# Optimization experiments

Measured on AMD Instinct MI355X. Metric: run time of the kernel, lower is better.

The kernel has to match this reference:

```python
import jax, jax.numpy as jnp
from jax import lax
import numpy as np

DN = ('NCDHW', 'OIDHW', 'NCDHW')


def _conv3(x, w, b):
    # standard 3x3x3 conv, stride 1, pad 1
    y = lax.conv_general_dilated(x, w, (1, 1, 1), ((1, 1), (1, 1), (1, 1)), dimension_numbers=DN)
    return y + b[None, :, None, None, None]


def _bn(x, gamma, beta, eps=1e-5):
    # training-mode batchnorm over (N, D, H, W), biased variance (torch semantics)
    mean = jnp.mean(x, axis=(0, 2, 3, 4), keepdims=True)
    var = jnp.var(x, axis=(0, 2, 3, 4), keepdims=True)
    return gamma[None, :, None, None, None] * (x - mean) * lax.rsqrt(var + eps) + beta[None, :, None, None, None]


def _deform_conv(x, off, w):
    # ConvOffset3d: one scalar offset per deformable group shifting the temporal (D)
    # sampling position of every kernel tap; linear interpolation along D, zero padding.
    N, C, D, H, W = x.shape
    G = off.shape[1]
    cpg = C // G
    offc = jnp.repeat(off, cpg, axis=1)                        # [N,C,D,H,W]
    base = offc + jnp.arange(D, dtype=x.dtype)[None, None, :, None, None]
    out = None
    for kd in range(3):                                        # 3 temporal taps
        pos = base + (kd - 1)                                  # fractional sample pos along D
        f0 = jnp.floor(pos)
        frac = pos - f0
        i0 = f0.astype(jnp.int32)
        i1 = i0 + 1
        m0 = ((i0 >= 0) & (i0 < D)).astype(x.dtype)
        m1 = ((i1 >= 0) & (i1 < D)).astype(x.dtype)
        g = (jnp.take_along_axis(x, jnp.clip(i0, 0, D - 1), axis=2) * ((1.0 - frac) * m0)
             + jnp.take_along_axis(x, jnp.clip(i1, 0, D - 1), axis=2) * (frac * m1))
        # the D-shift for tap kd is already baked into g -> conv with kernel (1,3,3)
        y = lax.conv_general_dilated(g, w[:, :, kd:kd + 1], (1, 1, 1), ((0, 0), (1, 1), (1, 1)), dimension_numbers=DN)
        out = y if out is None else out + y
    return out


def setup_inputs() -> dict:
    key = jax.random.key(0)
    ks = jax.random.split(key, 4)
    C, cpg = 64, 8
    N, D, H, W = 8, 16, 56, 56
    G = C // cpg
    s = 1.0 / np.sqrt(C * 27).astype(np.float32)
    x = jax.random.normal(ks[0], (N, C, D, H, W), jnp.float32)
    w_off = jax.random.normal(ks[1], (G, C, 3, 3, 3), jnp.float32) * s
    b_off = jnp.zeros((G,), jnp.float32)
    w1 = jax.random.normal(ks[2], (C, C, 3, 3, 3), jnp.float32) * s
    w2 = jax.random.normal(ks[3], (C, C, 3, 3, 3), jnp.float32) * s
    b2 = jnp.zeros((C,), jnp.float32)
    return dict(x=x, w_off=w_off, b_off=b_off, w1=w1, w2=w2, b2=b2,
                bn1_gamma=jnp.ones((C,), jnp.float32), bn1_beta=jnp.zeros((C,), jnp.float32),
                bn2_gamma=jnp.ones((C,), jnp.float32), bn2_beta=jnp.zeros((C,), jnp.float32))


def reference(x, w_off, b_off, w1, w2, b2, bn1_gamma, bn1_beta, bn2_gamma, bn2_beta):
    off = _conv3(x, w_off, b_off)               # [N, G, D, H, W]
    out = _deform_conv(x, off, w1)              # deformable conv (no bias)
    out = jax.nn.relu(_bn(out, bn1_gamma, bn1_beta))
    out = _conv3(out, w2, b2)
    out = _bn(out, bn2_gamma, bn2_beta) + x     # residual
    out = jax.nn.relu(out)
    return (out, off)
```

## Files before the change

kernel.cpp:

```cpp
#include <hip/hip_runtime.h>

#define HW 3136
#define DHW 50176
#define NEL 25690112
#define CNT 401408.0f

typedef __attribute__((ext_vector_type(8))) short          short8;
typedef __attribute__((ext_vector_type(8))) unsigned short ushort8;
typedef __attribute__((ext_vector_type(4))) float          f32x4;

__device__ __forceinline__ unsigned f2bf(float f) {
    union { float f; unsigned u; } v; v.f = f;
    return (v.u + 0x7FFFu + ((v.u >> 16) & 1u)) >> 16;
}
__device__ __forceinline__ float bf2f(unsigned u) {
    union { unsigned u; float f; } v; v.u = u << 16;
    return v.f;
}
__device__ __forceinline__ unsigned cvt_pk_bf16(float lo, float hi) {
    unsigned r;
    asm("v_cvt_pk_bf16_f32 %0, %1, %2" : "=v"(r) : "v"(lo), "v"(hi));
    return r;
}

__device__ __forceinline__ void xcd_decode(int& h, int& d, int& n) {
    const int bid = blockIdx.x + 56 * (blockIdx.y + 16 * blockIdx.z);
    const int swz = (bid & 7) * 896 + (bid >> 3);
    h = swz % 56;
    const int dn = swz / 56;
    d = dn & 15;
    n = dn >> 4;
}

__global__ __launch_bounds__(256) void k_transpose(
    const float* __restrict__ x, unsigned short* __restrict__ xt)
{
    __shared__ unsigned lds[4][64 * 36];
    const int d = blockIdx.x, n = blockIdx.y, z = blockIdx.z;
    const int wave = threadIdx.x >> 6, lane = threadIdx.x & 63;
    const float* xb = x + (size_t)n * 64 * DHW + d * HW;
    unsigned short* xtb = xt + (size_t)n * DHW * 64;
    unsigned* L = lds[wave];

    for (int c = z * 7 + wave; c < z * 7 + 7 && c < 49; c += 4) {
        const int P = c * 64;
#pragma unroll 4
        for (int cp = 0; cp < 32; ++cp) {
            const float a = xb[(size_t)(2 * cp) * DHW + P + lane];
            const float b = xb[(size_t)(2 * cp + 1) * DHW + P + lane];
            L[lane * 36 + cp] = cvt_pk_bf16(a, b);
        }
#pragma unroll
        for (int k = 0; k < 8; ++k) {
            const int r = (lane >> 3) + 8 * k;
            const uint4 v = *(const uint4*)&L[r * 36 + 4 * (lane & 7)];
            *(uint4*)((char*)xtb + ((size_t)(P + r) * 16 + d) * 128 + (lane & 7) * 16) = v;
        }
    }
}

__global__ __launch_bounds__(256) void k_wprep(
    const float* __restrict__ w_off, const float* __restrict__ w1,
    const float* __restrict__ w2, unsigned short* __restrict__ BtO,
    unsigned short* __restrict__ Bt1, unsigned short* __restrict__ Bt2)
{
    const int i = blockIdx.x * 256 + threadIdx.x;
    if (i < 27648) {
        const int tap = i / 1024, r = i - tap * 1024;
        const int ks = r >> 9, r3 = r & 511, lane = r3 >> 3, e = r3 & 7;
        const int row = lane & 15;
        const int ci  = ks * 32 + (lane >> 4) * 8 + e;
        BtO[i] = (row < 8) ? (unsigned short)f2bf(w_off[(row * 64 + ci) * 27 + tap]) : 0;
    }
    if (i < 110592) {
        const int tap = i / 4096, r = i - tap * 4096;
        const int rg = r >> 10, r2 = r & 1023;
        const int ks = r2 >> 9, r3 = r2 & 511, lane = r3 >> 3, e = r3 & 7;
        const int co = rg * 16 + (lane & 15);
        const int ci = ks * 32 + (lane >> 4) * 8 + e;
        Bt1[i] = (unsigned short)f2bf(w1[(co * 64 + ci) * 27 + tap]);
        Bt2[i] = (unsigned short)f2bf(w2[(co * 64 + ci) * 27 + tap]);
    }
}

template<int NCO, bool BN, bool DIN>
__global__ __launch_bounds__((NCO == 8) ? 256 : 512) void k_conv(
    const unsigned short* __restrict__ src, const unsigned short* __restrict__ Bt,
    const float* __restrict__ bias, const float* __restrict__ scv,
    const float* __restrict__ shv, float* __restrict__ dst)
{
    constexpr int NT = (NCO == 8) ? 256 : 512;
    __shared__ unsigned short A[538 * 72];
    int h, d, n;
    xcd_decode(h, d, n);
    const int tid = threadIdx.x;
    const int wave = tid >> 6, lane = tid & 63, lm = lane & 15, quad = lane >> 4;
    const int k8 = tid & 7;

    float scr[8], shr[8];
    if constexpr (BN) {
#pragma unroll
        for (int e = 0; e < 8; ++e) { scr[e] = scv[k8 * 8 + e]; shr[e] = shv[k8 * 8 + e]; }
    }

    const unsigned short* snb = DIN ? (src + (size_t)n * DHW * 64)
                                    : (src + (size_t)(n * 16) * HW * 64);

    for (int c = tid; c < 4176; c += NT) {
        const int idx = c >> 3;
        const int row = idx / 58, px = idx - row * 58;
        const int kd = row / 3, kh = row - kd * 3;
        const int dq = d + kd - 1, hq = h + kh - 1, wq = px - 1;
        uint4 pk = {0u, 0u, 0u, 0u};
        if (((unsigned)dq < 16u) & ((unsigned)hq < 56u) & ((unsigned)wq < 56u)) {
            const size_t off = DIN ? (((size_t)(hq * 56 + wq) * 16 + dq) * 64)
                                   : (((size_t)dq * HW + hq * 56 + wq) * 64);
            const ushort8 val = *(const ushort8*)(snb + off + k8 * 8);
            if constexpr (BN) {
                float f[8];
#pragma unroll
                for (int e = 0; e < 8; ++e)
                    f[e] = fmaxf(fmaf(bf2f(val[e]), scr[e], shr[e]), 0.f);
                pk.x = cvt_pk_bf16(f[0], f[1]);
                pk.y = cvt_pk_bf16(f[2], f[3]);
                pk.z = cvt_pk_bf16(f[4], f[5]);
                pk.w = cvt_pk_bf16(f[6], f[7]);
            } else {
                pk = *(const uint4*)&val;
            }
        }
        *(uint4*)&A[(size_t)idx * 72 + k8 * 8] = pk;
    }
    __syncthreads();

    constexpr int NFm = (NCO == 8) ? 1 : 2;
    const int mf0 = (NCO == 8) ? wave : (wave & 1) * 2;
    const int nf0 = (NCO == 8) ? 0 : (wave >> 1);

    f32x4 acc[NFm];
#pragma unroll
    for (int i = 0; i < NFm; ++i) acc[i] = (f32x4){0.f, 0.f, 0.f, 0.f};

    constexpr unsigned BSTR = (NCO == 8) ? 1024u : 4096u;
    const unsigned short* Btb = (NCO == 8) ? Bt : (Bt + (unsigned)nf0 * 1024);
    unsigned boff = (unsigned)lane * 8;
    short8 bc0 = *(const short8*)(Btb + boff);
    short8 bc1 = *(const short8*)(Btb + boff + 512);
    boff += BSTR;
    unsigned arow = (unsigned)(mf0 * 16 + lm) * 72 + quad * 8;

#pragma unroll 1
    for (int r9 = 0; r9 < 9; ++r9) {
#pragma unroll
        for (int kw = 0; kw < 3; ++kw) {
            const bool more = (kw < 2) | (r9 < 8);
            short8 bn0, bn1;
            if (more) {
                bn0 = *(const short8*)(Btb + boff);
                bn1 = *(const short8*)(Btb + boff + 512);
            }
            const unsigned ab = arow + kw * 72;
            short8 a0[NFm], a1[NFm];
#pragma unroll
            for (int mf = 0; mf < NFm; ++mf) {
                a0[mf] = *(const short8*)&A[ab + mf * 1152];
                a1[mf] = *(const short8*)&A[ab + mf * 1152 + 32];
            }
#pragma unroll
            for (int mf = 0; mf < NFm; ++mf)
                acc[mf] = __builtin_amdgcn_mfma_f32_16x16x32_bf16(a0[mf], bc0, acc[mf], 0, 0, 0);
#pragma unroll
            for (int mf = 0; mf < NFm; ++mf)
                acc[mf] = __builtin_amdgcn_mfma_f32_16x16x32_bf16(a1[mf], bc1, acc[mf], 0, 0, 0);
            if (more) {
                bc0 = bn0; bc1 = bn1;
                boff += BSTR;
            }
        }
        arow += 58 * 72;
    }

    __syncthreads();
    float* E = (float*)A;
    constexpr int CSTR = (NCO == 64) ? 65 : 17;
#pragma unroll
    for (int mf = 0; mf < NFm; ++mf)
#pragma unroll
        for (int r = 0; r < 4; ++r) {
            const int mm = (mf0 + mf) * 16 + quad * 4 + r;
            if (mm < 56) E[mm * CSTR + nf0 * 16 + lm] = acc[mf][r];
        }
    __syncthreads();
    for (int f = tid; f < 56 * NCO; f += NT) {
        const int co = f / 56, w0 = f - co * 56;
        dst[((size_t)(n * NCO + co) * 16 + d) * HW + h * 56 + w0] = E[w0 * CSTR + co] + bias[co];
    }
}

__global__ __launch_bounds__(512) void k_deform(
    const unsigned short* __restrict__ xt, const float* __restrict__ offo,
    const unsigned short* __restrict__ Bt, unsigned short* __restrict__ out1)
{
    __shared__ unsigned short A[538 * 72];
    int h, d, n;
    xcd_decode(h, d, n);
    const int tid = threadIdx.x;
    const int wave = tid >> 6, lane = tid & 63, lm = lane & 15, quad = lane >> 4;

    float pv[3];
#pragma unroll
    for (int it = 0; it < 3; ++it) {
        const int c = tid + it * 512;
        float p = 0.f;
        if (c < 1392) {
            const int g = c & 7, pix = c >> 3;
            const int hq3 = pix / 58, px = pix - hq3 * 58;
            const int habs = h + hq3 - 1, wq = px - 1;
            if (((unsigned)habs < 56u) & ((unsigned)wq < 56u))
                p = offo[((size_t)(n * 8 + g) * 16 + d) * HW + habs * 56 + wq] + (float)d;
        }
        pv[it] = p;
    }

#pragma unroll
    for (int it = 0; it < 3; ++it) {
        const int c = tid + it * 512;
        if (c >= 1392) break;
        const int g = c & 7, pix = c >> 3;
        const int hq3 = pix / 58, px = pix - hq3 * 58;
        const int habs = h + hq3 - 1, wq = px - 1;
        uint4 p0 = {0u,0u,0u,0u}, p1 = {0u,0u,0u,0u}, p2 = {0u,0u,0u,0u};
        if (((unsigned)habs < 56u) & ((unsigned)wq < 56u)) {
            const float p = pv[it];
            const float fl = floorf(p);
            const float fr = p - fl;
            const int i0 = (int)fl;
            const unsigned short* cb = xt + ((size_t)n * HW + habs * 56 + wq) * (16 * 64) + g * 8;
            float sv[4][8], m[4];
#pragma unroll
            for (int j = 0; j < 4; ++j) {
                const int dj = i0 - 1 + j;
                const bool ok = (unsigned)dj < 16u;
                m[j] = ok ? 1.f : 0.f;
                const ushort8 v = *(const ushort8*)(cb + (size_t)(ok ? dj : 0) * 64);
#pragma unroll
                for (int e = 0; e < 8; ++e) sv[j][e] = bf2f(v[e]);
            }
            const float fi = 1.f - fr;
            const float w0a = fi * m[0], w0b = fr * m[1];
            const float w1a = fi * m[1], w1b = fr * m[2];
            const float w2a = fi * m[2], w2b = fr * m[3];
            float a0[8], a1[8], a2[8];
#pragma unroll
            for (int e = 0; e < 8; ++e) {
                a0[e] = fmaf(sv[1][e], w0b, sv[0][e] * w0a);
                a1[e] = fmaf(sv[2][e], w1b, sv[1][e] * w1a);
                a2[e] = fmaf(sv[3][e], w2b, sv[2][e] * w2a);
            }
            p0.x = cvt_pk_bf16(a0[0], a0[1]); p0.y = cvt_pk_bf16(a0[2], a0[3]);
            p0.z = cvt_pk_bf16(a0[4], a0[5]); p0.w = cvt_pk_bf16(a0[6], a0[7]);
            p1.x = cvt_pk_bf16(a1[0], a1[1]); p1.y = cvt_pk_bf16(a1[2], a1[3]);
            p1.z = cvt_pk_bf16(a1[4], a1[5]); p1.w = cvt_pk_bf16(a1[6], a1[7]);
            p2.x = cvt_pk_bf16(a2[0], a2[1]); p2.y = cvt_pk_bf16(a2[2], a2[3]);
            p2.z = cvt_pk_bf16(a2[4], a2[5]); p2.w = cvt_pk_bf16(a2[6], a2[7]);
        }
        const int sl = hq3 * 58 + px;
        *(uint4*)&A[(size_t)(sl          ) * 72 + g * 8] = p0;
        *(uint4*)&A[(size_t)(sl + 3 * 58 ) * 72 + g * 8] = p1;
        *(uint4*)&A[(size_t)(sl + 6 * 58 ) * 72 + g * 8] = p2;
    }
    __syncthreads();

    const int mf0 = (wave & 1) * 2, nf0 = wave >> 1;
    f32x4 acc[2];
    acc[0] = (f32x4){0.f, 0.f, 0.f, 0.f};
    acc[1] = (f32x4){0.f, 0.f, 0.f, 0.f};

    const unsigned short* Btb = Bt + (unsigned)nf0 * 1024;
    unsigned boff = (unsigned)lane * 8;
    short8 bc0 = *(const short8*)(Btb + boff);
    short8 bc1 = *(const short8*)(Btb + boff + 512);
    boff += 4096u;
    unsigned arow = (unsigned)(mf0 * 16 + lm) * 72 + quad * 8;

#pragma unroll 1
    for (int r9 = 0; r9 < 9; ++r9) {
#pragma unroll
        for (int kw = 0; kw < 3; ++kw) {
            const bool more = (kw < 2) | (r9 < 8);
            short8 bn0, bn1;
            if (more) {
                bn0 = *(const short8*)(Btb + boff);
                bn1 = *(const short8*)(Btb + boff + 512);
            }
            const unsigned ab = arow + kw * 72;
            const short8 a00 = *(const short8*)&A[ab];
            const short8 a01 = *(const short8*)&A[ab + 1152];
            const short8 a10 = *(const short8*)&A[ab + 32];
            const short8 a11 = *(const short8*)&A[ab + 1152 + 32];
            acc[0] = __builtin_amdgcn_mfma_f32_16x16x32_bf16(a00, bc0, acc[0], 0, 0, 0);
            acc[1] = __builtin_amdgcn_mfma_f32_16x16x32_bf16(a01, bc0, acc[1], 0, 0, 0);
            acc[0] = __builtin_amdgcn_mfma_f32_16x16x32_bf16(a10, bc1, acc[0], 0, 0, 0);
            acc[1] = __builtin_amdgcn_mfma_f32_16x16x32_bf16(a11, bc1, acc[1], 0, 0, 0);
            if (more) {
                bc0 = bn0; bc1 = bn1;
                boff += 4096u;
            }
        }
        arow += 58 * 72;
    }

    __syncthreads();
#pragma unroll
    for (int mf = 0; mf < 2; ++mf)
#pragma unroll
        for (int r = 0; r < 4; ++r) {
            const int mm = (mf0 + mf) * 16 + quad * 4 + r;
            if (mm < 56)
                A[mm * 72 + nf0 * 16 + lm] = (unsigned short)f2bf(acc[mf][r]);
        }
    __syncthreads();
    const size_t pixb = ((size_t)(n * 16) + d) * HW + h * 56;
    if (tid < 448) {
        const int px = tid >> 3, kk = tid & 7;
        *(uint4*)(out1 + (pixb + px) * 64 + kk * 8) = *(const uint4*)&A[px * 72 + kk * 8];
    }
}

__global__ __launch_bounds__(256) void k_stats_bf16(
    const unsigned short* __restrict__ src, float* __restrict__ sums, float* __restrict__ sqs)
{
    const int c4 = threadIdx.x & 15, part = threadIdx.x >> 4;
    const size_t base = (size_t)blockIdx.x * 1024;
    float s[4] = {0.f, 0.f, 0.f, 0.f}, q[4] = {0.f, 0.f, 0.f, 0.f};
#pragma unroll 4
    for (int i = 0; i < 64; ++i) {
        const size_t pix = base + part + (size_t)i * 16;
        const uint2 v = *(const uint2*)(src + pix * 64 + c4 * 4);
        const float f0 = bf2f(v.x & 0xffffu), f1 = bf2f(v.x >> 16);
        const float f2 = bf2f(v.y & 0xffffu), f3 = bf2f(v.y >> 16);
        s[0] += f0; q[0] = fmaf(f0, f0, q[0]);
        s[1] += f1; q[1] = fmaf(f1, f1, q[1]);
        s[2] += f2; q[2] = fmaf(f2, f2, q[2]);
        s[3] += f3; q[3] = fmaf(f3, f3, q[3]);
    }
    __shared__ float S[64], Q[64];
    if (threadIdx.x < 64) { S[threadIdx.x] = 0.f; Q[threadIdx.x] = 0.f; }
    __syncthreads();
#pragma unroll
    for (int e = 0; e < 4; ++e) {
        atomicAdd(&S[c4 * 4 + e], s[e]);
        atomicAdd(&Q[c4 * 4 + e], q[e]);
    }
    __syncthreads();
    if (threadIdx.x < 64) {
        atomicAdd(&sums[threadIdx.x], S[threadIdx.x]);
        atomicAdd(&sqs[threadIdx.x],  Q[threadIdx.x]);
    }
}

__global__ __launch_bounds__(256) void k_stats(
    const float* __restrict__ src, float* __restrict__ sums, float* __restrict__ sqs)
{
    const int c = blockIdx.x, n = blockIdx.y;
    const float* p = src + ((size_t)n * 64 + c) * DHW;
    float s = 0.f, q = 0.f;
    for (int i = threadIdx.x; i < DHW; i += 256) {
        const float v = p[i];
        s += v; q = fmaf(v, v, q);
    }
    for (int o = 32; o > 0; o >>= 1) {
        s += __shfl_down(s, o);
        q += __shfl_down(q, o);
    }
    __shared__ float ls[4], lq[4];
    const int wv = threadIdx.x >> 6, lane = threadIdx.x & 63;
    if (lane == 0) { ls[wv] = s; lq[wv] = q; }
    __syncthreads();
    if (threadIdx.x == 0) {
        atomicAdd(&sums[c], ls[0] + ls[1] + ls[2] + ls[3]);
        atomicAdd(&sqs[c],  lq[0] + lq[1] + lq[2] + lq[3]);
    }
}

__global__ void k_finalize(const float* __restrict__ sums, const float* __restrict__ sqs,
                           const float* __restrict__ gamma, const float* __restrict__ beta,
                           float* __restrict__ scale, float* __restrict__ shift)
{
    const int c = threadIdx.x;
    const float mean = sums[c] / CNT;
    const float var  = sqs[c] / CNT - mean * mean;
    const float sc   = gamma[c] * rsqrtf(var + 1e-5f);
    scale[c] = sc;
    shift[c] = fmaf(-mean, sc, beta[c]);
}

__global__ __launch_bounds__(256) void k_residual(
    float4* __restrict__ dst, const float4* __restrict__ raw,
    const float4* __restrict__ x,
    const float* __restrict__ scale, const float* __restrict__ shift)
{
    const int i = blockIdx.x * 256 + threadIdx.x;
    const int c = (i / 12544) & 63;
    const float sc = scale[c], sh = shift[c];
    float4 v = raw[i];
    const float4 xv = x[i];
    v.x = fmaxf(fmaf(v.x, sc, sh) + xv.x, 0.f);
    v.y = fmaxf(fmaf(v.y, sc, sh) + xv.y, 0.f);
    v.z = fmaxf(fmaf(v.z, sc, sh) + xv.z, 0.f);
    v.w = fmaxf(fmaf(v.w, sc, sh) + xv.w, 0.f);
    dst[i] = v;
}

extern "C" void kernel_launch(void* const* d_in, const int* in_sizes, int n_in,
                              void* d_out, int out_size, void* d_ws, size_t ws_size,
                              hipStream_t stream) {
    const float* x     = (const float*)d_in[0];
    const float* w_off = (const float*)d_in[1];
    const float* b_off = (const float*)d_in[2];
    const float* w1    = (const float*)d_in[3];
    const float* w2    = (const float*)d_in[4];
    const float* b2    = (const float*)d_in[5];
    const float* g1    = (const float*)d_in[6];
    const float* be1   = (const float*)d_in[7];
    const float* g2    = (const float*)d_in[8];
    const float* be2   = (const float*)d_in[9];

    float* out     = (float*)d_out;
    float* off_out = out + NEL;
    unsigned short* out1 = (unsigned short*)d_out;
    unsigned short* wb   = (unsigned short*)(out + 13000000);
    unsigned short* BtO  = wb;
    unsigned short* Bt1  = BtO + 27648;
    unsigned short* Bt2  = Bt1 + 110592;

    unsigned short* xt  = (unsigned short*)d_ws;
    float*          raw = (float*)d_ws;
    float*          st  = (float*)d_ws + NEL;

    hipMemsetAsync(st, 0, 512 * sizeof(float), stream);

    k_transpose<<<dim3(16, 8, 7), 256, 0, stream>>>(x, xt);
    k_wprep<<<432, 256, 0, stream>>>(w_off, w1, w2, BtO, Bt1, Bt2);

    const dim3 cgrid(56, 16, 8);
    k_conv<8, false, true><<<cgrid, 256, 0, stream>>>(xt, BtO, b_off, nullptr, nullptr, off_out);
    k_deform<<<cgrid, 512, 0, stream>>>(xt, off_out, Bt1, out1);

    k_stats_bf16<<<392, 256, 0, stream>>>(out1, st + 0, st + 64);
    k_finalize<<<1, 64, 0, stream>>>(st + 0, st + 64, g1, be1, st + 128, st + 192);

    k_conv<64, true, false><<<cgrid, 512, 0, stream>>>(out1, Bt2, b2, st + 128, st + 192, raw);

    k_stats<<<dim3(64, 8), 256, 0, stream>>>(raw, st + 256, st + 320);
    k_finalize<<<1, 64, 0, stream>>>(st + 256, st + 320, g2, be2, st + 384, st + 448);
    k_residual<<<25088, 256, 0, stream>>>((float4*)out, (const float4*)raw, (const float4*)x, st + 384, st + 448);
}
```

Before: 751.9 us.

## Fuse batchnorm statistics into conv epilogues and split offset-conv K across waves

Removes the separate k_stats_bf16 and k_stats passes by computing per-channel sums and sums of squares in the epilogues of the deformable conv and the second conv. Each epilogue reduces over 8 lanes with shuffles and then does global atomics. The offset conv now runs with 512 threads and splits the K dimension across two wave groups, summing the two partials through shared memory. The tile load loop is also rewritten into a fixed 9-row unrolled pattern. This saves two full reads of the large intermediates, at the cost of many more global atomics and a slightly different floating-point summation order.

```diff
diff --git a/kernel.cpp b/kernel.cpp
--- a/kernel.cpp
+++ b/kernel.cpp
@@ -84,12 +84,12 @@
 }
 
 template<int NCO, bool BN, bool DIN>
-__global__ __launch_bounds__((NCO == 8) ? 256 : 512) void k_conv(
+__global__ __launch_bounds__(512) void k_conv(
     const unsigned short* __restrict__ src, const unsigned short* __restrict__ Bt,
     const float* __restrict__ bias, const float* __restrict__ scv,
-    const float* __restrict__ shv, float* __restrict__ dst)
-{
-    constexpr int NT = (NCO == 8) ? 256 : 512;
+    const float* __restrict__ shv, float* __restrict__ dst,
+    float* __restrict__ osum, float* __restrict__ osq)
+{
     __shared__ unsigned short A[538 * 72];
     int h, d, n;
     xcd_decode(h, d, n);
@@ -106,13 +106,15 @@
     const unsigned short* snb = DIN ? (src + (size_t)n * DHW * 64)
                                     : (src + (size_t)(n * 16) * HW * 64);
 
-    for (int c = tid; c < 4176; c += NT) {
-        const int idx = c >> 3;
-        const int row = idx / 58, px = idx - row * 58;
-        const int kd = row / 3, kh = row - kd * 3;
-        const int dq = d + kd - 1, hq = h + kh - 1, wq = px - 1;
+    const int spx = tid >> 3;
+    const int wq  = spx - 1;
+    const bool pxok = (tid < 464) & ((unsigned)wq < 56u);
+#pragma unroll
+    for (int row = 0; row < 9; ++row) {
+        const int kd = row / 3, kh = row - (row / 3) * 3;
+        const int dq = d + kd - 1, hq = h + kh - 1;
         uint4 pk = {0u, 0u, 0u, 0u};
-        if (((unsigned)dq < 16u) & ((unsigned)hq < 56u) & ((unsigned)wq < 56u)) {
+        if (pxok & ((unsigned)dq < 16u) & ((unsigned)hq < 56u)) {
             const size_t off = DIN ? (((size_t)(hq * 56 + wq) * 16 + dq) * 64)
                                    : (((size_t)dq * HW + hq * 56 + wq) * 64);
             const ushort8 val = *(const ushort8*)(snb + off + k8 * 8);
@@ -129,77 +131,115 @@
                 pk = *(const uint4*)&val;
             }
         }
-        *(uint4*)&A[(size_t)idx * 72 + k8 * 8] = pk;
+        if (tid < 464) *(uint4*)&A[(size_t)(row * 58 + spx) * 72 + k8 * 8] = pk;
     }
     __syncthreads();
 
-    constexpr int NFm = (NCO == 8) ? 1 : 2;
-    const int mf0 = (NCO == 8) ? wave : (wave & 1) * 2;
-    const int nf0 = (NCO == 8) ? 0 : (wave >> 1);
-
-    f32x4 acc[NFm];
-#pragma unroll
-    for (int i = 0; i < NFm; ++i) acc[i] = (f32x4){0.f, 0.f, 0.f, 0.f};
-
-    constexpr unsigned BSTR = (NCO == 8) ? 1024u : 4096u;
-    const unsigned short* Btb = (NCO == 8) ? Bt : (Bt + (unsigned)nf0 * 1024);
-    unsigned boff = (unsigned)lane * 8;
-    short8 bc0 = *(const short8*)(Btb + boff);
-    short8 bc1 = *(const short8*)(Btb + boff + 512);
-    boff += BSTR;
-    unsigned arow = (unsigned)(mf0 * 16 + lm) * 72 + quad * 8;
-
+    if constexpr (NCO == 8) {
+        const int ksw = wave >> 2, mf = wave & 3;
+        f32x4 acc = (f32x4){0.f, 0.f, 0.f, 0.f};
+        const unsigned short* Btb = Bt + ksw * 512;
+        unsigned boff = (unsigned)lane * 8;
+        short8 bc = *(const short8*)(Btb + boff);
+        boff += 1024u;
+        unsigned arow = (unsigned)(mf * 16 + lm) * 72 + quad * 8 + ksw * 32;
 #pragma unroll 1
-    for (int r9 = 0; r9 < 9; ++r9) {
-#pragma unroll
-        for (int kw = 0; kw < 3; ++kw) {
-            const bool more = (kw < 2) | (r9 < 8);
-            short8 bn0, bn1;
-            if (more) {
-                bn0 = *(const short8*)(Btb + boff);
-                bn1 = *(const short8*)(Btb + boff + 512);
-            }
-            const unsigned ab = arow + kw * 72;
-            short8 a0[NFm], a1[NFm];
-#pragma unroll
-            for (int mf = 0; mf < NFm; ++mf) {
-                a0[mf] = *(const short8*)&A[ab + mf * 1152];
-                a1[mf] = *(const short8*)&A[ab + mf * 1152 + 32];
-            }
-#pragma unroll
-            for (int mf = 0; mf < NFm; ++mf)
-                acc[mf] = __builtin_amdgcn_mfma_f32_16x16x32_bf16(a0[mf], bc0, acc[mf], 0, 0, 0);
-#pragma unroll
-            for (int mf = 0; mf < NFm; ++mf)
-                acc[mf] = __builtin_amdgcn_mfma_f32_16x16x32_bf16(a1[mf], bc1, acc[mf], 0, 0, 0);
-            if (more) {
-                bc0 = bn0; bc1 = bn1;
-                boff += BSTR;
-            }
-        }
-        arow += 58 * 72;
-    }
-
-    __syncthreads();
-    float* E = (float*)A;
-    constexpr int CSTR = (NCO == 64) ? 65 : 17;
-#pragma unroll
-    for (int mf = 0; mf < NFm; ++mf)
+        for (int r9 = 0; r9 < 9; ++r9) {
+#pragma unroll
+            for (int kw = 0; kw < 3; ++kw) {
+                const bool more = (kw < 2) | (r9 < 8);
+                short8 bn;
+                if (more) bn = *(const short8*)(Btb + boff);
+                const short8 a = *(const short8*)&A[arow + kw * 72];
+                acc = __builtin_amdgcn_mfma_f32_16x16x32_bf16(a, bc, acc, 0, 0, 0);
+                if (more) { bc = bn; boff += 1024u; }
+            }
+            arow += 58 * 72;
+        }
+        __syncthreads();
+        float* E = (float*)A;
 #pragma unroll
         for (int r = 0; r < 4; ++r) {
-            const int mm = (mf0 + mf) * 16 + quad * 4 + r;
-            if (mm < 56) E[mm * CSTR + nf0 * 16 + lm] = acc[mf][r];
-        }
-    __syncthreads();
-    for (int f = tid; f < 56 * NCO; f += NT) {
-        const int co = f / 56, w0 = f - co * 56;
-        dst[((size_t)(n * NCO + co) * 16 + d) * HW + h * 56 + w0] = E[w0 * CSTR + co] + bias[co];
+            const int mm = mf * 16 + quad * 4 + r;
+            if (mm < 56) E[ksw * 952 + mm * 17 + lm] = acc[r];
+        }
+        __syncthreads();
+        if (lane < 56) {
+            const float v = E[lane * 17 + wave] + E[952 + lane * 17 + wave] + bias[wave];
+            dst[((size_t)(n * 8 + wave) * 16 + d) * HW + h * 56 + lane] = v;
+        }
+    } else {
+        const int mf0 = (wave & 1) * 2, nf0 = wave >> 1;
+        f32x4 acc[2];
+        acc[0] = (f32x4){0.f, 0.f, 0.f, 0.f};
+        acc[1] = (f32x4){0.f, 0.f, 0.f, 0.f};
+
+        const unsigned short* Btb = Bt + (unsigned)nf0 * 1024;
+        unsigned boff = (unsigned)lane * 8;
+        short8 bc0 = *(const short8*)(Btb + boff);
+        short8 bc1 = *(const short8*)(Btb + boff + 512);
+        boff += 4096u;
+        unsigned arow = (unsigned)(mf0 * 16 + lm) * 72 + quad * 8;
+
+#pragma unroll 1
+        for (int r9 = 0; r9 < 9; ++r9) {
+#pragma unroll
+            for (int kw = 0; kw < 3; ++kw) {
+                const bool more = (kw < 2) | (r9 < 8);
+                short8 bn0, bn1;
+                if (more) {
+                    bn0 = *(const short8*)(Btb + boff);
+                    bn1 = *(const short8*)(Btb + boff + 512);
+                }
+                const unsigned ab = arow + kw * 72;
+                const short8 a00 = *(const short8*)&A[ab];
+                const short8 a01 = *(const short8*)&A[ab + 1152];
+                const short8 a10 = *(const short8*)&A[ab + 32];
+                const short8 a11 = *(const short8*)&A[ab + 1152 + 32];
+                acc[0] = __builtin_amdgcn_mfma_f32_16x16x32_bf16(a00, bc0, acc[0], 0, 0, 0);
+                acc[1] = __builtin_amdgcn_mfma_f32_16x16x32_bf16(a01, bc0, acc[1], 0, 0, 0);
+                acc[0] = __builtin_amdgcn_mfma_f32_16x16x32_bf16(a10, bc1, acc[0], 0, 0, 0);
+                acc[1] = __builtin_amdgcn_mfma_f32_16x16x32_bf16(a11, bc1, acc[1], 0, 0, 0);
+                if (more) { bc0 = bn0; bc1 = bn1; boff += 4096u; }
+            }
+            arow += 58 * 72;
+        }
+
+        __syncthreads();
+        float* E = (float*)A;
+#pragma unroll
+        for (int mf = 0; mf < 2; ++mf)
+#pragma unroll
+            for (int r = 0; r < 4; ++r) {
+                const int mm = (mf0 + mf) * 16 + quad * 4 + r;
+                if (mm < 56) E[mm * 65 + nf0 * 16 + lm] = acc[mf][r];
+            }
+        __syncthreads();
+        const int co = tid >> 3, w8 = tid & 7;
+        const float bco = bias[co];
+        float* drow = &dst[((size_t)(n * 64 + co) * 16 + d) * HW + h * 56];
+        float s = 0.f, q = 0.f;
+#pragma unroll
+        for (int i = 0; i < 7; ++i) {
+            const int w0 = w8 + 8 * i;
+            const float v = E[w0 * 65 + co] + bco;
+            drow[w0] = v;
+            s += v; q = fmaf(v, v, q);
+        }
+        s += __shfl_down(s, 1); q += __shfl_down(q, 1);
+        s += __shfl_down(s, 2); q += __shfl_down(q, 2);
+        s += __shfl_down(s, 4); q += __shfl_down(q, 4);
+        if ((lane & 7) == 0) {
+            atomicAdd(&osum[co], s);
+            atomicAdd(&osq[co],  q);
+        }
     }
 }
 
 __global__ __launch_bounds__(512) void k_deform(
     const unsigned short* __restrict__ xt, const float* __restrict__ offo,
-    const unsigned short* __restrict__ Bt, unsigned short* __restrict__ out1)
+    const unsigned short* __restrict__ Bt, unsigned short* __restrict__ out1,
+    float* __restrict__ osum, float* __restrict__ osq)
 {
     __shared__ unsigned short A[538 * 72];
     int h, d, n;
@@ -302,10 +342,7 @@
             acc[1] = __builtin_amdgcn_mfma_f32_16x16x32_bf16(a01, bc0, acc[1], 0, 0, 0);
             acc[0] = __builtin_amdgcn_mfma_f32_16x16x32_bf16(a10, bc1, acc[0], 0, 0, 0);
             acc[1] = __builtin_amdgcn_mfma_f32_16x16x32_bf16(a11, bc1, acc[1], 0, 0, 0);
-            if (more) {
-                bc0 = bn0; bc1 = bn1;
-                boff += 4096u;
-            }
+            if (more) { bc0 = bn0; bc1 = bn1; boff += 4096u; }
         }
         arow += 58 * 72;
     }
@@ -325,61 +362,20 @@
         const int px = tid >> 3, kk = tid & 7;
         *(uint4*)(out1 + (pixb + px) * 64 + kk * 8) = *(const uint4*)&A[px * 72 + kk * 8];
     }
-}
-
-__global__ __launch_bounds__(256) void k_stats_bf16(
-    const unsigned short* __restrict__ src, float* __restrict__ sums, float* __restrict__ sqs)
-{
-    const int c4 = threadIdx.x & 15, part = threadIdx.x >> 4;
-    const size_t base = (size_t)blockIdx.x * 1024;
-    float s[4] = {0.f, 0.f, 0.f, 0.f}, q[4] = {0.f, 0.f, 0.f, 0.f};
-#pragma unroll 4
-    for (int i = 0; i < 64; ++i) {
-        const size_t pix = base + part + (size_t)i * 16;
-        const uint2 v = *(const uint2*)(src + pix * 64 + c4 * 4);
-        const float f0 = bf2f(v.x & 0xffffu), f1 = bf2f(v.x >> 16);
-        const float f2 = bf2f(v.y & 0xffffu), f3 = bf2f(v.y >> 16);
-        s[0] += f0; q[0] = fmaf(f0, f0, q[0]);
-        s[1] += f1; q[1] = fmaf(f1, f1, q[1]);
-        s[2] += f2; q[2] = fmaf(f2, f2, q[2]);
-        s[3] += f3; q[3] = fmaf(f3, f3, q[3]);
-    }
-    __shared__ float S[64], Q[64];
-    if (threadIdx.x < 64) { S[threadIdx.x] = 0.f; Q[threadIdx.x] = 0.f; }
-    __syncthreads();
-#pragma unroll
-    for (int e = 0; e < 4; ++e) {
-        atomicAdd(&S[c4 * 4 + e], s[e]);
-        atomicAdd(&Q[c4 * 4 + e], q[e]);
-    }
-    __syncthreads();
-    if (threadIdx.x < 64) {
-        atomicAdd(&sums[threadIdx.x], S[threadIdx.x]);
-        atomicAdd(&sqs[threadIdx.x],  Q[threadIdx.x]);
-    }
-}
-
-__global__ __launch_bounds__(256) void k_stats(
-    const float* __restrict__ src, float* __restrict__ sums, float* __restrict__ sqs)
-{
-    const int c = blockIdx.x, n = blockIdx.y;
-    const float* p = src + ((size_t)n * 64 + c) * DHW;
+    const int co = tid >> 3, w8 = tid & 7;
     float s = 0.f, q = 0.f;
-    for (int i = threadIdx.x; i < DHW; i += 256) {
-        const float v = p[i];
+#pragma unroll
+    for (int i = 0; i < 7; ++i) {
+        const int w0 = w8 + 8 * i;
+        const float v = bf2f(A[w0 * 72 + co]);
         s += v; q = fmaf(v, v, q);
     }
-    for (int o = 32; o > 0; o >>= 1) {
-        s += __shfl_down(s, o);
-        q += __shfl_down(q, o);
-    }
-    __shared__ float ls[4], lq[4];
-    const int wv = threadIdx.x >> 6, lane = threadIdx.x & 63;
-    if (lane == 0) { ls[wv] = s; lq[wv] = q; }
-    __syncthreads();
-    if (threadIdx.x == 0) {
-        atomicAdd(&sums[c], ls[0] + ls[1] + ls[2] + ls[3]);
-        atomicAdd(&sqs[c],  lq[0] + lq[1] + lq[2] + lq[3]);
+    s += __shfl_down(s, 1); q += __shfl_down(q, 1);
+    s += __shfl_down(s, 2); q += __shfl_down(q, 2);
+    s += __shfl_down(s, 4); q += __shfl_down(q, 4);
+    if ((lane & 7) == 0) {
+        atomicAdd(&osum[co], s);
+        atomicAdd(&osq[co],  q);
     }
 }
 
@@ -444,15 +440,13 @@
     k_wprep<<<432, 256, 0, stream>>>(w_off, w1, w2, BtO, Bt1, Bt2);
 
     const dim3 cgrid(56, 16, 8);
-    k_conv<8, false, true><<<cgrid, 256, 0, stream>>>(xt, BtO, b_off, nullptr, nullptr, off_out);
-    k_deform<<<cgrid, 512, 0, stream>>>(xt, off_out, Bt1, out1);
-
-    k_stats_bf16<<<392, 256, 0, stream>>>(out1, st + 0, st + 64);
+    k_conv<8, false, true><<<cgrid, 512, 0, stream>>>(xt, BtO, b_off, nullptr, nullptr, off_out, nullptr, nullptr);
+    k_deform<<<cgrid, 512, 0, stream>>>(xt, off_out, Bt1, out1, st + 0, st + 64);
+
     k_finalize<<<1, 64, 0, stream>>>(st + 0, st + 64, g1, be1, st + 128, st + 192);
 
-    k_conv<64, true, false><<<cgrid, 512, 0, stream>>>(out1, Bt2, b2, st + 128, st + 192, raw);
-
-    k_stats<<<dim3(64, 8), 256, 0, stream>>>(raw, st + 256, st + 320);
+    k_conv<64, true, false><<<cgrid, 512, 0, stream>>>(out1, Bt2, b2, st + 128, st + 192, raw, st + 256, st + 320);
+
     k_finalize<<<1, 64, 0, stream>>>(st + 256, st + 320, g2, be2, st + 384, st + 448);
     k_residual<<<25088, 256, 0, stream>>>((float4*)out, (const float4*)raw, (const float4*)x, st + 384, st + 448);
 }
```

New measurement: 1.066 ms. 41.7% more time.
